# Optimization experiments

Measured on AMD Instinct MI355X. Metric: run time of the kernel, lower is better.

## Reference

```python
import jax, jax.numpy as jnp
import numpy as np

S = 7          # grid cells per side (CFG['CELL_NUMS'])
L_COORD = 5.0  # CFG['L_COORD']
L_NOOBJ = 0.5  # CFG['L_NOOBJ']
N_BATCH = 16384


def setup_inputs() -> dict:
    key = jax.random.key(0)
    k1, k2, k3 = jax.random.split(key, 3)
    pred = jax.random.uniform(k1, (N_BATCH, S, S, 30), dtype=jnp.float32)
    target = jax.random.uniform(k2, (N_BATCH, S, S, 30), dtype=jnp.float32)
    obj = jax.random.uniform(k3, (N_BATCH, S, S)) < 0.3
    target = target.at[..., 4].set(jnp.where(obj, target[..., 4], 0.0))
    target = target.at[..., 9].set(jnp.where(obj, target[..., 9], 0.0))
    return {"pred_tensor": pred, "target_tensor": target}


def _yolo_v1_loss(pred, target):
    # pred/target: [N, S, S, 30] = [2 boxes x (x,y,w,h,c), 20 class probs]
    N = pred.shape[0]
    coo_f = (target[..., 4] > 0).astype(pred.dtype)   # [N,S,S] object cells
    noo_f = 1.0 - coo_f                                # no-object cells

    # no-object loss: confidence channels 4 and 9 on noo cells (sum-MSE)
    nooobj_loss = jnp.sum(
        noo_f * ((pred[..., 4] - target[..., 4]) ** 2
                 + (pred[..., 9] - target[..., 9]) ** 2))

    # class loss over object cells (sum-MSE over 20 classes)
    class_loss = jnp.sum(coo_f[..., None] * (pred[..., 10:] - target[..., 10:]) ** 2)

    # boxes: [N,S,S,2,5]
    pb = pred[..., :10].reshape(N, S, S, 2, 5)
    tb = target[..., :10].reshape(N, S, S, 2, 5)

    # xywh -> xyxy for the 2 predicted boxes and the first target box per cell
    p_lt = pb[..., :2] - 0.5 * pb[..., 2:4]
    p_rb = pb[..., :2] + 0.5 * pb[..., 2:4]
    t0 = tb[..., 0, :]                                 # target box used for IOU
    t_lt = t0[..., :2] - 0.5 * t0[..., 2:4]
    t_rb = t0[..., :2] + 0.5 * t0[..., 2:4]

    # NOTE: faithful reproduction of the source's compute_iou, including its
    # bug: wh = (rb - lt < 0).float(), so 'inter' is an indicator product.
    lt = jnp.maximum(p_lt, t_lt[..., None, :])         # [N,S,S,2,2]
    rb = jnp.minimum(p_rb, t_rb[..., None, :])
    wh_ind = (rb - lt < 0).astype(pred.dtype)
    inter = wh_ind[..., 0] * wh_ind[..., 1]            # [N,S,S,2]
    area1 = (p_rb[..., 0] - p_lt[..., 0]) * (p_rb[..., 1] - p_lt[..., 1])
    area2 = ((t_rb[..., 0] - t_lt[..., 0]) * (t_rb[..., 1] - t_lt[..., 1]))[..., None]
    iou = inter / (area1 + area2 - inter)              # [N,S,S,2]

    # responsible box = argmax IOU over the 2 predicted boxes per cell
    idx = jnp.argmax(iou, axis=-1)                     # [N,S,S]
    gather = idx[..., None, None]                      # [N,S,S,1,1]
    resp_p = jnp.take_along_axis(pb, gather, axis=3)[..., 0, :]  # [N,S,S,5]
    resp_t = jnp.take_along_axis(tb, gather, axis=3)[..., 0, :]

    contain_loss = jnp.sum(coo_f * (resp_p[..., 4] - resp_t[..., 4]) ** 2)

    # guard sqrt at masked-out cells so 0*d(sqrt(0)) does not produce NaN grads
    safe = coo_f[..., None] > 0
    sqrt_wp = jnp.sqrt(jnp.where(safe, resp_p[..., 2:4], 1.0))
    sqrt_wt = jnp.sqrt(jnp.where(safe, resp_t[..., 2:4], 1.0))
    loc_loss = (jnp.sum(coo_f[..., None] * (resp_p[..., :2] - resp_t[..., :2]) ** 2)
                + jnp.sum(coo_f[..., None] * (sqrt_wp - sqrt_wt) ** 2))

    return (L_COORD * loc_loss + contain_loss + L_NOOBJ * nooobj_loss + class_loss) / N


def reference(pred_tensor, target_tensor):
    return _yolo_v1_loss(pred_tensor, target_tensor)
```

## Files before the change

kernel.cpp:

```cpp
#include <hip/hip_runtime.h>


#define CH 30
#define CPB 64
#define T 64
#define TILE_F (CPB * CH)
#define TILE_V4 (TILE_F / 4)

typedef __attribute__((address_space(3))) void* lds_vp;
typedef const __attribute__((address_space(1))) void* gvp;

__global__ __launch_bounds__(T, 2)
void yolo_partial(const float* __restrict__ pred,
                  const float* __restrict__ targ,
                  float* __restrict__ partial) {
    __shared__ float tile[2 * TILE_F];

    const int tid = threadIdx.x;
    const long long fbase = (long long)blockIdx.x * TILE_F;

    const float4* gt = (const float4*)(targ + fbase);
    const float4* gp = (const float4*)(pred + fbase);
#pragma unroll
    for (int k = 0; k < 8; ++k) {
        const int v = tid + k * T;
        if (v < TILE_V4)
            __builtin_amdgcn_global_load_lds((gvp)(gt + v), (lds_vp)(tile + 4 * v),
                                             16, 0, 0);
    }
#pragma unroll
    for (int k = 0; k < 8; ++k) {
        const int v = tid + k * T;
        if (v < TILE_V4)
            __builtin_amdgcn_global_load_lds((gvp)(gp + v),
                                             (lds_vp)(tile + TILE_F + 4 * v),
                                             16, 0, 0);
    }
    __syncthreads();

    float sum;
    {
        const float2* t2 = (const float2*)(tile + tid * CH);
        const float2* p2 = (const float2*)(tile + TILE_F + tid * CH);
        float2 t[15], p[15];
#pragma unroll
        for (int k = 0; k < 15; ++k) t[k] = t2[k];
#pragma unroll
        for (int k = 0; k < 15; ++k) p[k] = p2[k];

        const float t4 = t[2].x, t9 = t[4].y;
        const bool coo = t4 > 0.0f;

        const float d4 = p[2].x - t4;
        const float d9 = p[4].y - t9;
        sum = coo ? 0.0f : 0.5f * (d4 * d4 + d9 * d9);

        if (coo) {
            float cl = 0.0f;
#pragma unroll
            for (int k = 0; k < 10; ++k) {
                const float dx = p[5 + k].x - t[5 + k].x;
                const float dy = p[5 + k].y - t[5 + k].y;
                cl += dx * dx + dy * dy;
            }
            sum += cl;

            const float tltx = t[0].x - 0.5f * t[1].x;
            const float tlty = t[0].y - 0.5f * t[1].y;
            const float trbx = t[0].x + 0.5f * t[1].x;
            const float trby = t[0].y + 0.5f * t[1].y;
            const float area2 = (trbx - tltx) * (trby - tlty);

            const float b0x = p[0].x, b0y = p[0].y, b0w = p[1].x, b0h = p[1].y;
            const float b1x = p[2].y, b1y = p[3].x, b1w = p[3].y, b1h = p[4].x;

            float iou0, iou1;
            {
                const float pltx = b0x - 0.5f * b0w, plty = b0y - 0.5f * b0h;
                const float prbx = b0x + 0.5f * b0w, prby = b0y + 0.5f * b0h;
                const float ltx = fmaxf(pltx, tltx), lty = fmaxf(plty, tlty);
                const float rbx = fminf(prbx, trbx), rby = fminf(prby, trby);
                const float inter = ((rbx - ltx < 0.0f) ? 1.0f : 0.0f) *
                                    ((rby - lty < 0.0f) ? 1.0f : 0.0f);
                const float area1 = (prbx - pltx) * (prby - plty);
                iou0 = inter / (area1 + area2 - inter);
            }
            {
                const float pltx = b1x - 0.5f * b1w, plty = b1y - 0.5f * b1h;
                const float prbx = b1x + 0.5f * b1w, prby = b1y + 0.5f * b1h;
                const float ltx = fmaxf(pltx, tltx), lty = fmaxf(plty, tlty);
                const float rbx = fminf(prbx, trbx), rby = fminf(prby, trby);
                const float inter = ((rbx - ltx < 0.0f) ? 1.0f : 0.0f) *
                                    ((rby - lty < 0.0f) ? 1.0f : 0.0f);
                const float area1 = (prbx - pltx) * (prby - plty);
                iou1 = inter / (area1 + area2 - inter);
            }
            const bool idx1 = iou1 > iou0;

            const float rpx = idx1 ? b1x : b0x;
            const float rpy = idx1 ? b1y : b0y;
            const float rpw = idx1 ? b1w : b0w;
            const float rph = idx1 ? b1h : b0h;
            const float rpc = idx1 ? p[4].y : p[2].x;
            const float rtx = idx1 ? t[2].y : t[0].x;
            const float rty = idx1 ? t[3].x : t[0].y;
            const float rtw = idx1 ? t[3].y : t[1].x;
            const float rth = idx1 ? t[4].x : t[1].y;
            const float rtc = idx1 ? t[4].y : t[2].x;

            const float dc = rpc - rtc;
            sum += dc * dc;

            const float dx = rpx - rtx;
            const float dy = rpy - rty;
            const float dw = sqrtf(rpw) - sqrtf(rtw);
            const float dh = sqrtf(rph) - sqrtf(rth);
            sum += 5.0f * (dx * dx + dy * dy + dw * dw + dh * dh);
        }
    }

#pragma unroll
    for (int off = 32; off > 0; off >>= 1)
        sum += __shfl_down(sum, off, 64);
    if (tid == 0) partial[blockIdx.x] = sum;
}

__global__ __launch_bounds__(256)
void yolo_reduce(const float* __restrict__ partial, int n, float* __restrict__ out) {
    __shared__ float wave_sums[4];
    float s = 0.0f;
    const int n4 = n >> 2;
    const float4* p4 = (const float4*)partial;
    for (int v = threadIdx.x; v < n4; v += 256) {
        const float4 x = p4[v];
        s += (x.x + x.y) + (x.z + x.w);
    }
    for (int v = (n4 << 2) + threadIdx.x; v < n; v += 256)
        s += partial[v];
#pragma unroll
    for (int off = 32; off > 0; off >>= 1)
        s += __shfl_down(s, off, 64);
    const int wave = threadIdx.x >> 6;
    const int lane = threadIdx.x & 63;
    if (lane == 0) wave_sums[wave] = s;
    __syncthreads();
    if (threadIdx.x == 0) {
        const float tot = wave_sums[0] + wave_sums[1] + wave_sums[2] + wave_sums[3];
        out[0] = tot * (1.0f / 16384.0f);
    }
}

extern "C" void kernel_launch(void* const* d_in, const int* in_sizes, int n_in,
                              void* d_out, int out_size, void* d_ws, size_t ws_size,
                              hipStream_t stream) {
    const float* pred = (const float*)d_in[0];
    const float* targ = (const float*)d_in[1];
    float* out = (float*)d_out;
    float* partial = (float*)d_ws;

    const int n_cells = in_sizes[0] / CH;
    const int blocks = n_cells / CPB;

    yolo_partial<<<blocks, T, 0, stream>>>(pred, targ, partial);
    yolo_reduce<<<1, 256, 0, stream>>>(partial, blocks, out);
}
```

Baseline: 204.4 us.

## Use persistent grid with double-buffered async LDS tile loads

Replaces the one-tile-per-block launch with a fixed grid of 1280 single-wave blocks. Each block walks over tiles with a stride of the grid size. Two LDS buffers are filled with global_load_lds, and s_waitcnt vmcnt/lgkmcnt sequencing lets the next tile's loads overlap computation on the current tile. This removes per-block launch and drain overhead and keeps more memory requests in flight per wave. The cost is relying on hand-counted vmcnt values and running fewer resident waves per CU.

```diff
diff --git a/kernel.cpp b/kernel.cpp
--- a/kernel.cpp
+++ b/kernel.cpp
@@ -2,127 +2,153 @@
 
 
 #define CH 30
-#define CPB 64
+#define CPT 64
 #define T 64
-#define TILE_F (CPB * CH)
+#define TILE_F (CPT * CH)
 #define TILE_V4 (TILE_F / 4)
+#define GRID 1280
 
 typedef __attribute__((address_space(3))) void* lds_vp;
 typedef const __attribute__((address_space(1))) void* gvp;
 
-__global__ __launch_bounds__(T, 2)
+__device__ __forceinline__ float cell_loss(const float* __restrict__ tb,
+                                           const float* __restrict__ pb) {
+    const float2* t2 = (const float2*)tb;
+    const float2* p2 = (const float2*)pb;
+    float2 t[15], p[15];
+#pragma unroll
+    for (int k = 0; k < 15; ++k) t[k] = t2[k];
+#pragma unroll
+    for (int k = 0; k < 15; ++k) p[k] = p2[k];
+
+    const float t4 = t[2].x, t9 = t[4].y;
+    const bool coo = t4 > 0.0f;
+
+    const float d4 = p[2].x - t4;
+    const float d9 = p[4].y - t9;
+    float sum = coo ? 0.0f : 0.5f * (d4 * d4 + d9 * d9);
+
+    if (coo) {
+        float cl = 0.0f;
+#pragma unroll
+        for (int k = 0; k < 10; ++k) {
+            const float dx = p[5 + k].x - t[5 + k].x;
+            const float dy = p[5 + k].y - t[5 + k].y;
+            cl += dx * dx + dy * dy;
+        }
+        sum += cl;
+
+        const float tltx = t[0].x - 0.5f * t[1].x;
+        const float tlty = t[0].y - 0.5f * t[1].y;
+        const float trbx = t[0].x + 0.5f * t[1].x;
+        const float trby = t[0].y + 0.5f * t[1].y;
+        const float area2 = (trbx - tltx) * (trby - tlty);
+
+        const float b0x = p[0].x, b0y = p[0].y, b0w = p[1].x, b0h = p[1].y;
+        const float b1x = p[2].y, b1y = p[3].x, b1w = p[3].y, b1h = p[4].x;
+
+        float iou0, iou1;
+        {
+            const float pltx = b0x - 0.5f * b0w, plty = b0y - 0.5f * b0h;
+            const float prbx = b0x + 0.5f * b0w, prby = b0y + 0.5f * b0h;
+            const float ltx = fmaxf(pltx, tltx), lty = fmaxf(plty, tlty);
+            const float rbx = fminf(prbx, trbx), rby = fminf(prby, trby);
+            const float inter = ((rbx - ltx < 0.0f) ? 1.0f : 0.0f) *
+                                ((rby - lty < 0.0f) ? 1.0f : 0.0f);
+            const float area1 = (prbx - pltx) * (prby - plty);
+            iou0 = inter / (area1 + area2 - inter);
+        }
+        {
+            const float pltx = b1x - 0.5f * b1w, plty = b1y - 0.5f * b1h;
+            const float prbx = b1x + 0.5f * b1w, prby = b1y + 0.5f * b1h;
+            const float ltx = fmaxf(pltx, tltx), lty = fmaxf(plty, tlty);
+            const float rbx = fminf(prbx, trbx), rby = fminf(prby, trby);
+            const float inter = ((rbx - ltx < 0.0f) ? 1.0f : 0.0f) *
+                                ((rby - lty < 0.0f) ? 1.0f : 0.0f);
+            const float area1 = (prbx - pltx) * (prby - plty);
+            iou1 = inter / (area1 + area2 - inter);
+        }
+        const bool idx1 = iou1 > iou0;
+
+        const float rpx = idx1 ? b1x : b0x;
+        const float rpy = idx1 ? b1y : b0y;
+        const float rpw = idx1 ? b1w : b0w;
+        const float rph = idx1 ? b1h : b0h;
+        const float rpc = idx1 ? p[4].y : p[2].x;
+        const float rtx = idx1 ? t[2].y : t[0].x;
+        const float rty = idx1 ? t[3].x : t[0].y;
+        const float rtw = idx1 ? t[3].y : t[1].x;
+        const float rth = idx1 ? t[4].x : t[1].y;
+        const float rtc = idx1 ? t[4].y : t[2].x;
+
+        const float dc = rpc - rtc;
+        sum += dc * dc;
+
+        const float dx = rpx - rtx;
+        const float dy = rpy - rty;
+        const float dw = sqrtf(rpw) - sqrtf(rtw);
+        const float dh = sqrtf(rph) - sqrtf(rth);
+        sum += 5.0f * (dx * dx + dy * dy + dw * dw + dh * dh);
+    }
+    return sum;
+}
+
+__global__ __launch_bounds__(T)
 void yolo_partial(const float* __restrict__ pred,
                   const float* __restrict__ targ,
-                  float* __restrict__ partial) {
-    __shared__ float tile[2 * TILE_F];
+                  float* __restrict__ partial, int ntiles) {
+    __shared__ float buf0[2 * TILE_F];
+    __shared__ float buf1[2 * TILE_F];
 
     const int tid = threadIdx.x;
-    const long long fbase = (long long)blockIdx.x * TILE_F;
+    const int bid = blockIdx.x;
 
-    const float4* gt = (const float4*)(targ + fbase);
-    const float4* gp = (const float4*)(pred + fbase);
+    const int nt = (bid < ntiles) ? ((ntiles - bid + GRID - 1) / GRID) : 0;
+
+    auto stage = [&](float* dst, int t) {
+        const float4* gt = (const float4*)targ + (long long)t * TILE_V4;
+        const float4* gp = (const float4*)pred + (long long)t * TILE_V4;
 #pragma unroll
-    for (int k = 0; k < 8; ++k) {
-        const int v = tid + k * T;
-        if (v < TILE_V4)
-            __builtin_amdgcn_global_load_lds((gvp)(gt + v), (lds_vp)(tile + 4 * v),
-                                             16, 0, 0);
-    }
+        for (int k = 0; k < 8; ++k) {
+            const int v = tid + k * T;
+            if (v < TILE_V4)
+                __builtin_amdgcn_global_load_lds((gvp)(gt + v),
+                                                 (lds_vp)(dst + 4 * v), 16, 0, 0);
+        }
 #pragma unroll
-    for (int k = 0; k < 8; ++k) {
-        const int v = tid + k * T;
-        if (v < TILE_V4)
-            __builtin_amdgcn_global_load_lds((gvp)(gp + v),
-                                             (lds_vp)(tile + TILE_F + 4 * v),
-                                             16, 0, 0);
-    }
-    __syncthreads();
+        for (int k = 0; k < 8; ++k) {
+            const int v = tid + k * T;
+            if (v < TILE_V4)
+                __builtin_amdgcn_global_load_lds((gvp)(gp + v),
+                                                 (lds_vp)(dst + TILE_F + 4 * v),
+                                                 16, 0, 0);
+        }
+    };
 
-    float sum;
-    {
-        const float2* t2 = (const float2*)(tile + tid * CH);
-        const float2* p2 = (const float2*)(tile + TILE_F + tid * CH);
-        float2 t[15], p[15];
-#pragma unroll
-        for (int k = 0; k < 15; ++k) t[k] = t2[k];
-#pragma unroll
-        for (int k = 0; k < 15; ++k) p[k] = p2[k];
+    float acc = 0.0f;
+    if (nt > 0) stage(buf0, bid);
+    if (nt > 1) stage(buf1, bid + GRID);
 
-        const float t4 = t[2].x, t9 = t[4].y;
-        const bool coo = t4 > 0.0f;
-
-        const float d4 = p[2].x - t4;
-        const float d9 = p[4].y - t9;
-        sum = coo ? 0.0f : 0.5f * (d4 * d4 + d9 * d9);
-
-        if (coo) {
-            float cl = 0.0f;
-#pragma unroll
-            for (int k = 0; k < 10; ++k) {
-                const float dx = p[5 + k].x - t[5 + k].x;
-                const float dy = p[5 + k].y - t[5 + k].y;
-                cl += dx * dx + dy * dy;
-            }
-            sum += cl;
-
-            const float tltx = t[0].x - 0.5f * t[1].x;
-            const float tlty = t[0].y - 0.5f * t[1].y;
-            const float trbx = t[0].x + 0.5f * t[1].x;
-            const float trby = t[0].y + 0.5f * t[1].y;
-            const float area2 = (trbx - tltx) * (trby - tlty);
-
-            const float b0x = p[0].x, b0y = p[0].y, b0w = p[1].x, b0h = p[1].y;
-            const float b1x = p[2].y, b1y = p[3].x, b1w = p[3].y, b1h = p[4].x;
-
-            float iou0, iou1;
-            {
-                const float pltx = b0x - 0.5f * b0w, plty = b0y - 0.5f * b0h;
-                const float prbx = b0x + 0.5f * b0w, prby = b0y + 0.5f * b0h;
-                const float ltx = fmaxf(pltx, tltx), lty = fmaxf(plty, tlty);
-                const float rbx = fminf(prbx, trbx), rby = fminf(prby, trby);
-                const float inter = ((rbx - ltx < 0.0f) ? 1.0f : 0.0f) *
-                                    ((rby - lty < 0.0f) ? 1.0f : 0.0f);
-                const float area1 = (prbx - pltx) * (prby - plty);
-                iou0 = inter / (area1 + area2 - inter);
-            }
-            {
-                const float pltx = b1x - 0.5f * b1w, plty = b1y - 0.5f * b1h;
-                const float prbx = b1x + 0.5f * b1w, prby = b1y + 0.5f * b1h;
-                const float ltx = fmaxf(pltx, tltx), lty = fmaxf(plty, tlty);
-                const float rbx = fminf(prbx, trbx), rby = fminf(prby, trby);
-                const float inter = ((rbx - ltx < 0.0f) ? 1.0f : 0.0f) *
-                                    ((rby - lty < 0.0f) ? 1.0f : 0.0f);
-                const float area1 = (prbx - pltx) * (prby - plty);
-                iou1 = inter / (area1 + area2 - inter);
-            }
-            const bool idx1 = iou1 > iou0;
-
-            const float rpx = idx1 ? b1x : b0x;
-            const float rpy = idx1 ? b1y : b0y;
-            const float rpw = idx1 ? b1w : b0w;
-            const float rph = idx1 ? b1h : b0h;
-            const float rpc = idx1 ? p[4].y : p[2].x;
-            const float rtx = idx1 ? t[2].y : t[0].x;
-            const float rty = idx1 ? t[3].x : t[0].y;
-            const float rtw = idx1 ? t[3].y : t[1].x;
-            const float rth = idx1 ? t[4].x : t[1].y;
-            const float rtc = idx1 ? t[4].y : t[2].x;
-
-            const float dc = rpc - rtc;
-            sum += dc * dc;
-
-            const float dx = rpx - rtx;
-            const float dy = rpy - rty;
-            const float dw = sqrtf(rpw) - sqrtf(rtw);
-            const float dh = sqrtf(rph) - sqrtf(rth);
-            sum += 5.0f * (dx * dx + dy * dy + dw * dw + dh * dh);
+    for (int k = 0; k < nt; ++k) {
+        if ((k & 1) == 0) {
+            if (k + 1 < nt) asm volatile("s_waitcnt vmcnt(16)" ::: "memory");
+            else            asm volatile("s_waitcnt vmcnt(0)"  ::: "memory");
+            acc += cell_loss(buf0 + tid * CH, buf0 + TILE_F + tid * CH);
+            asm volatile("s_waitcnt lgkmcnt(0)" ::: "memory");
+            if (k + 2 < nt) stage(buf0, bid + (k + 2) * GRID);
+        } else {
+            if (k + 1 < nt) asm volatile("s_waitcnt vmcnt(16)" ::: "memory");
+            else            asm volatile("s_waitcnt vmcnt(0)"  ::: "memory");
+            acc += cell_loss(buf1 + tid * CH, buf1 + TILE_F + tid * CH);
+            asm volatile("s_waitcnt lgkmcnt(0)" ::: "memory");
+            if (k + 2 < nt) stage(buf1, bid + (k + 2) * GRID);
         }
     }
 
 #pragma unroll
     for (int off = 32; off > 0; off >>= 1)
-        sum += __shfl_down(sum, off, 64);
-    if (tid == 0) partial[blockIdx.x] = sum;
+        acc += __shfl_down(acc, off, 64);
+    if (tid == 0) partial[bid] = acc;
 }
 
 __global__ __launch_bounds__(256)
@@ -159,8 +185,8 @@
     float* partial = (float*)d_ws;
 
     const int n_cells = in_sizes[0] / CH;
-    const int blocks = n_cells / CPB;
+    const int ntiles = n_cells / CPT;
 
-    yolo_partial<<<blocks, T, 0, stream>>>(pred, targ, partial);
-    yolo_reduce<<<1, 256, 0, stream>>>(partial, blocks, out);
+    yolo_partial<<<GRID, T, 0, stream>>>(pred, targ, partial, ntiles);
+    yolo_reduce<<<1, 256, 0, stream>>>(partial, GRID, out);
 }
```

Result: no change. 204.6 us (+0.1%).
